# Kernel optimization log

Measured on AMD Instinct MI355X. Metric: run time of the kernel, lower is better.

## Reference

```python
import jax, jax.numpy as jnp
import numpy as np

# model dims
B, S, R, D = 2, 64, 2048, 1024      # batch, num_bars(summary len), reg seq len, embed dim
H, KVH, HD = 16, 4, 64              # q heads, kv heads, head dim
G = H // KVH                        # GQA group size
KVD = KVH * HD
TPB = R // S                        # tokens per bar = 32
SCALE = HD ** -0.5
NEG = -1e9


def _rotate_half(x):
    x1, x2 = jnp.split(x, 2, axis=-1)
    return jnp.concatenate([-x2, x1], axis=-1)


def _apply_rope(q, k, cos, sin):
    return q * cos + _rotate_half(q) * sin, k * cos + _rotate_half(k) * sin


def _rope_1d(seq_len):
    # standard RoPE tables, shape (1, 1, seq_len, HD)
    inv = 1.0 / (10000.0 ** (jnp.arange(0, HD, 2, dtype=jnp.float32) / HD))
    freqs = jnp.arange(seq_len, dtype=jnp.float32)[:, None] * inv
    emb = jnp.concatenate([freqs, freqs], axis=-1)
    return jnp.cos(emb)[None, None], jnp.sin(emb)[None, None]


def _rope_2d(bar_ids, tib):
    # hierarchical 2D RoPE: half the rotary freqs encode bar id, half encode token-in-bar id
    q4 = HD // 4
    inv = 1.0 / (10000.0 ** (jnp.arange(q4, dtype=jnp.float32) * 2.0 / (HD // 2)))
    fb = bar_ids.astype(jnp.float32)[..., None] * inv   # (B, R, HD/4)
    ft = tib.astype(jnp.float32)[..., None] * inv       # (B, R, HD/4)
    freqs = jnp.concatenate([fb, ft], axis=-1)          # (B, R, HD/2)
    emb = jnp.concatenate([freqs, freqs], axis=-1)      # (B, R, HD)
    return jnp.cos(emb)[:, None], jnp.sin(emb)[:, None]


def _attn(q, k, v, mask):
    # masked softmax attention; mask (Lq, Lk) broadcast over batch/heads
    s = jnp.einsum('bhqd,bhkd->bhqk', q, k) * SCALE
    s = jnp.where(mask[None, None], s, NEG)
    p = jax.nn.softmax(s, axis=-1)
    return jnp.einsum('bhqk,bhkd->bhqd', p, v)


def _lin(x, w, b):
    return x @ w + b


def _heads(x, n):
    b, l, _ = x.shape
    return x.reshape(b, l, n, HD).transpose(0, 2, 1, 3)


def _merge(x):
    b, h, l, _ = x.shape
    return x.transpose(0, 2, 1, 3).reshape(b, l, h * HD)


PARAM_SHAPES = [('w_sq', (D, D)), ('b_sq', (D,)), ('w_sk', (D, KVD)), ('b_sk', (KVD,)),
                ('w_sv', (D, KVD)), ('b_sv', (KVD,)), ('w_so', (D, D)), ('b_so', (D,)),
                ('w_rq', (D, D)), ('b_rq', (D,)), ('w_rk', (D, KVD)), ('b_rk', (KVD,)),
                ('w_rv', (D, KVD)), ('b_rv', (KVD,)), ('w_ro', (D, D)), ('b_ro', (D,)),
                ('w_k2', (D, KVD)), ('b_k2', (KVD,)), ('w_v2', (D, KVD)), ('b_v2', (KVD,))]


def setup_inputs() -> dict:
    key = jax.random.key(0)
    ks = jax.random.split(key, 2 + len(PARAM_SHAPES))
    inp = {}
    inp['sum_x'] = jax.random.normal(ks[0], (B, S, D), jnp.float32)
    inp['reg_x'] = jax.random.normal(ks[1], (B, R, D), jnp.float32)
    for i, (n, shp) in enumerate(PARAM_SHAPES):
        inp[n] = jax.random.normal(ks[2 + i], shp, jnp.float32) * 0.02
    pos = jnp.arange(R)
    bar = pos // TPB
    tib = pos % TPB
    inp['bar_ids'] = jnp.tile(bar[None], (B, 1)).astype(jnp.int32)
    inp['token_in_bar_ids'] = jnp.tile(tib[None], (B, 1)).astype(jnp.int32)
    # summarize phase: summary-bar i attends to summary j<=i and regular tokens in bars<=i
    key_bar = jnp.concatenate([jnp.arange(S), bar])
    inp['summarize_block_mask'] = key_bar[None, :] <= jnp.arange(S)[:, None]
    # updating phase: regular token t attends to summary-K2 of bars<=bar(t) and regular s<=t
    upd = jnp.concatenate([jnp.arange(S)[None, :] <= bar[:, None],
                           pos[None, :] <= pos[:, None]], axis=1)
    inp['updating_block_mask'] = upd
    return inp


def reference(sum_x, reg_x, w_sq, b_sq, w_sk, b_sk, w_sv, b_sv, w_so, b_so,
              w_rq, b_rq, w_rk, b_rk, w_rv, b_rv, w_ro, b_ro, w_k2, b_k2, w_v2, b_v2,
              summarize_block_mask, updating_block_mask, bar_ids, token_in_bar_ids):
    sum_q = _heads(_lin(sum_x, w_sq, b_sq), H)
    sum_k = _heads(_lin(sum_x, w_sk, b_sk), KVH)
    sum_v = _heads(_lin(sum_x, w_sv, b_sv), KVH)
    reg_q = _heads(_lin(reg_x, w_rq, b_rq), H)
    reg_k = _heads(_lin(reg_x, w_rk, b_rk), KVH)
    reg_v = _heads(_lin(reg_x, w_rv, b_rv), KVH)
    # 1D RoPE for summary tokens, 2D hierarchical RoPE for regular tokens
    cos, sin = _rope_1d(S)
    sum_q, sum_k = _apply_rope(sum_q, sum_k, cos, sin)
    rcos, rsin = _rope_2d(bar_ids, token_in_bar_ids)
    reg_q, reg_k = _apply_rope(reg_q, reg_k, rcos, rsin)
    rep = lambda t: jnp.repeat(t, G, axis=1)  # GQA repeat_interleave over heads
    reg_k_r, reg_v_r = rep(reg_k), rep(reg_v)
    # phase 1: summarize (summary queries over [summary; regular] keys)
    cat_k = jnp.concatenate([rep(sum_k), reg_k_r], axis=2)
    cat_v = jnp.concatenate([rep(sum_v), reg_v_r], axis=2)
    sum_attn = _merge(_attn(sum_q, cat_k, cat_v, summarize_block_mask))  # (B, S, D)
    # phase 2: updating (regular queries over [summary K2/V2; regular] keys)
    k2 = rep(_heads(_lin(sum_attn, w_k2, b_k2), KVH))
    v2 = rep(_heads(_lin(sum_attn, w_v2, b_v2), KVH))
    cat_k2 = jnp.concatenate([k2, reg_k_r], axis=2)
    cat_v2 = jnp.concatenate([v2, reg_v_r], axis=2)
    reg_attn = _merge(_attn(reg_q, cat_k2, cat_v2, updating_block_mask))  # (B, R, D)
    return _lin(sum_attn, w_so, b_so), _lin(reg_attn, w_ro, b_ro)
```

## Files before the change

### kernel.cpp

```cpp
#include <hip/hip_runtime.h>

typedef unsigned short u16;
typedef __attribute__((ext_vector_type(8))) short s8v;
typedef __attribute__((ext_vector_type(4))) float f4v;

#define B_    2
#define S_    64
#define R_    2048
#define D_    1024
#define H_    16
#define KVH_  4
#define LOG2_10K 13.287712379549449f
#define QSC_  0.18033688011112042f

__device__ __forceinline__ u16 f2bf(float f) {
  union { float f; unsigned int i; } v; v.f = f;
  unsigned int x = v.i;
  return (u16)((x + 0x7FFFu + ((x >> 16) & 1u)) >> 16);
}
__device__ __forceinline__ u16 f2bf_ru(float f) {
  union { float f; unsigned int i; } v; v.f = f;
  return (u16)((v.i + 0x8000u) >> 16);
}

struct WT10 { const float* w[10]; u16* o[10]; int C[10]; };

__global__ __launch_bounds__(256)
void transw_k(WT10 ws)
{
  const int z = blockIdx.z;
  const int C = ws.C[z];
  const int c0 = blockIdx.x * 32, k0 = blockIdx.y * 32;
  if (c0 >= C) return;
  __shared__ float t[32][33];
  const float* w = ws.w[z];
  u16* o = ws.o[z];
  const int x = threadIdx.x & 31, y = threadIdx.x >> 5;
  #pragma unroll
  for (int j = 0; j < 4; j++)
    t[y + 8 * j][x] = w[(size_t)(k0 + y + 8 * j) * C + c0 + x];
  __syncthreads();
  #pragma unroll
  for (int j = 0; j < 4; j++)
    o[(size_t)(c0 + y + 8 * j) * 1024 + k0 + x] = f2bf(t[x][y + 8 * j]);
}

__global__ __launch_bounds__(256)
void convx_k(const float* __restrict__ xa, const float* __restrict__ xb,
             u16* __restrict__ oa, u16* __restrict__ ob)
{
  int i = (blockIdx.x * 256 + threadIdx.x) * 8;
  const float* src; u16* dst; int off;
  if (i < 131072) { src = xa; dst = oa; off = i; }
  else            { src = xb; dst = ob; off = i - 131072; }
  float4 a = *(const float4*)(src + off);
  float4 b = *(const float4*)(src + off + 4);
  s8v r;
  r[0] = (short)f2bf(a.x); r[1] = (short)f2bf(a.y);
  r[2] = (short)f2bf(a.z); r[3] = (short)f2bf(a.w);
  r[4] = (short)f2bf(b.x); r[5] = (short)f2bf(b.y);
  r[6] = (short)f2bf(b.z); r[7] = (short)f2bf(b.w);
  *(s8v*)(dst + off) = r;
}

__device__ __forceinline__ void gemm_core_db(
    const u16* __restrict__ Xrow, const u16* __restrict__ WTrow,
    u16 (*Adb)[72], u16 (*Bdb)[72], f4v (&acc)[2][4],
    int tid, int l15, int l4, int wro, int wco)
{
  s8v pa[2], pb[2];
  #pragma unroll
  for (int it = 0; it < 2; it++) {
    int seg = tid + it * 512;
    int r = seg >> 3, sg = (seg & 7) * 8;
    pa[it] = *(const s8v*)(Xrow  + (size_t)r * 1024 + sg);
    pb[it] = *(const s8v*)(WTrow + (size_t)r * 1024 + sg);
  }
  #pragma unroll
  for (int it = 0; it < 2; it++) {
    int seg = tid + it * 512;
    int r = seg >> 3, sg = (seg & 7) * 8;
    *(s8v*)&Adb[r][sg] = pa[it];
    *(s8v*)&Bdb[r][sg] = pb[it];
  }
  __syncthreads();

  #pragma unroll 2
  for (int k = 0; k < 16; k++) {
    const int off = (k & 1) * 128;
    if (k + 1 < 16) {
      const int k0 = (k + 1) * 64;
      #pragma unroll
      for (int it = 0; it < 2; it++) {
        int seg = tid + it * 512;
        int r = seg >> 3, sg = (seg & 7) * 8;
        pa[it] = *(const s8v*)(Xrow  + (size_t)r * 1024 + k0 + sg);
        pb[it] = *(const s8v*)(WTrow + (size_t)r * 1024 + k0 + sg);
      }
    }
    s8v af[2][2], bf4[4][2];
    #pragma unroll
    for (int rc = 0; rc < 2; rc++) {
      af[rc][0] = *(const s8v*)&Adb[off + wro + rc * 16 + l15][l4 * 8];
      af[rc][1] = *(const s8v*)&Adb[off + wro + rc * 16 + l15][32 + l4 * 8];
    }
    #pragma unroll
    for (int cc = 0; cc < 4; cc++) {
      bf4[cc][0] = *(const s8v*)&Bdb[off + wco + cc * 16 + l15][l4 * 8];
      bf4[cc][1] = *(const s8v*)&Bdb[off + wco + cc * 16 + l15][32 + l4 * 8];
    }
    #pragma unroll
    for (int rc = 0; rc < 2; rc++)
      #pragma unroll
      for (int cc = 0; cc < 4; cc++) {
        acc[rc][cc] = __builtin_amdgcn_mfma_f32_16x16x32_bf16(af[rc][0], bf4[cc][0], acc[rc][cc], 0, 0, 0);
        acc[rc][cc] = __builtin_amdgcn_mfma_f32_16x16x32_bf16(af[rc][1], bf4[cc][1], acc[rc][cc], 0, 0, 0);
      }
    if (k + 1 < 16) {
      const int noff = ((k + 1) & 1) * 128;
      #pragma unroll
      for (int it = 0; it < 2; it++) {
        int seg = tid + it * 512;
        int r = seg >> 3, sg = (seg & 7) * 8;
        *(s8v*)&Adb[noff + r][sg] = pa[it];
        *(s8v*)&Bdb[noff + r][sg] = pb[it];
      }
    }
    __syncthreads();
  }
}

__device__ __forceinline__ void epi_to_lds(
    const f4v (&acc)[2][4], const float* __restrict__ Bp, u16* __restrict__ Es,
    int cbr, int wro, int wco, int grb, int LB,
    int ropeMode, bool rope2d, bool sc, int l15, int l4)
{
  float bv[4];
  #pragma unroll
  for (int cc = 0; cc < 4; cc++) bv[cc] = Bp[cbr + cc * 16 + l15];

  if (ropeMode == 0) {
    #pragma unroll
    for (int rc = 0; rc < 2; rc++)
      #pragma unroll
      for (int reg = 0; reg < 4; reg++) {
        int lrow = wro + rc * 16 + l4 * 4 + reg;
        #pragma unroll
        for (int cc = 0; cc < 4; cc++)
          Es[lrow * 136 + wco + cc * 16 + l15] = f2bf(acc[rc][cc][reg] + bv[cc]);
      }
  } else {
    float step = rope2d ? (LOG2_10K / 16.f) : (LOG2_10K / 32.f);
    float inv_lo = exp2f(-(float)l15 * step);
    float inv_hi = rope2d ? inv_lo : inv_lo * exp2f(-16.f * step);
    #pragma unroll
    for (int rc = 0; rc < 2; rc++)
      #pragma unroll
      for (int reg = 0; reg < 4; reg++) {
        int lrow = wro + rc * 16 + l4 * 4 + reg;
        int grow = grb + lrow;
        int pos = grow & (LB - 1);
        int bar = pos >> 5, tib = pos & 31;
        #pragma unroll
        for (int cc = 0; cc < 4; cc++) {
          float inv = (cc & 1) ? inv_hi : inv_lo;
          float bse = rope2d ? (float)((cc & 1) ? tib : bar) : (float)pos;
          float ang = bse * inv;
          float sn, cs;
          sincosf(ang, &sn, &cs);
          float v0 = acc[rc][cc][reg] + bv[cc];
          float v1 = acc[rc][cc ^ 2][reg] + bv[cc ^ 2];
          float rot = (cc < 2) ? -v1 : v1;
          float val = v0 * cs + rot * sn;
          if (sc) val *= QSC_;
          Es[lrow * 136 + wco + cc * 16 + l15] = f2bf(val);
        }
      }
  }
}

__device__ __forceinline__ void store_tile_bf16(
    const u16* __restrict__ Es, u16* __restrict__ out,
    int grb, int c0r, int NH, int LB, int LBS, int tid)
{
  #pragma unroll
  for (int it = 0; it < 4; it++) {
    int idx = it * 512 + tid;
    int r = idx >> 4, ch = idx & 15;
    int grow = grb + r;
    int b = grow >> LBS, pos = grow & (LB - 1);
    int cg = c0r + ch * 8;
    size_t base = (((size_t)b * NH + (cg >> 6)) * LB + pos) * 64 + (cg & 63);
    *(s8v*)(out + base) = *(const s8v*)(Es + r * 136 + ch * 8);
  }
}

__device__ __forceinline__ void store_tile_vT(
    const u16* __restrict__ Es, u16* __restrict__ outT,
    int grb, int kvbase, int LB, int LBS, int tid)
{
  #pragma unroll
  for (int it = 0; it < 4; it++) {
    int idx = tid + it * 512;
    int dcol = idx & 127, rg = idx >> 7;
    int grow = grb + rg * 8;
    int b = grow >> LBS, pos = grow & (LB - 1);
    u16 tmp[8];
    #pragma unroll
    for (int j = 0; j < 8; j++) tmp[j] = Es[(rg * 8 + j) * 136 + dcol];
    u16* dst = outT + (((size_t)(b * KVH_ + kvbase + (dcol >> 6))) * 64 + (dcol & 63)) * LB + pos;
    *(s8v*)dst = *(s8v*)tmp;
  }
}

struct QkvA {
  const u16 *X, *WTs, *WTr;
  const float *b0s, *b1s, *b2s, *b0r, *b1r, *b2r;
  u16 *o0s, *o1s, *o2s, *o0r, *o1r, *o2r;
};

__global__ __launch_bounds__(512)
void qkv_k(QkvA a)
{
  int orig = blockIdx.x;
  int xcd = orig & 7, sidx = orig >> 3;
  int wg = (xcd < 4) ? (xcd * 50 + sidx) : (200 + (xcd - 4) * 49 + sidx);
  const int bx = wg % 12, by = wg / 12;
  const bool issum = (by == 0);
  const int c0 = bx * 128;

  __shared__ u16 Adb[256][72];
  __shared__ u16 Bdb[256][72];
  u16* Es = &Adb[0][0];

  const int tid  = threadIdx.x;
  const int lane = tid & 63;
  const int w    = tid >> 6;
  const int l15  = lane & 15;
  const int l4   = lane >> 4;
  const int wro  = (w >> 1) * 32;
  const int wco  = (w & 1) * 64;

  f4v acc[2][4];
  #pragma unroll
  for (int i = 0; i < 2; i++)
    #pragma unroll
    for (int j = 0; j < 4; j++) acc[i][j] = (f4v){0.f, 0.f, 0.f, 0.f};

  const u16* Xrow  = a.X + (size_t)by * 128 * 1024;
  const u16* WTrow = (issum ? a.WTs : a.WTr) + (size_t)c0 * 1024;
  gemm_core_db(Xrow, WTrow, Adb, Bdb, acc, tid, l15, l4, wro, wco);

  const int LB  = issum ? 64 : 2048;
  const int LBS = issum ? 6 : 11;
  const int grb = issum ? 0 : (by - 1) * 128;

  if (c0 < 1024) {
    epi_to_lds(acc, issum ? a.b0s : a.b0r, Es, c0 + wco, wro, wco, grb, LB, 1, !issum, true, l15, l4);
    __syncthreads();
    store_tile_bf16(Es, issum ? a.o0s : a.o0r, grb, c0, 16, LB, LBS, tid);
  } else if (c0 < 1280) {
    epi_to_lds(acc, issum ? a.b1s : a.b1r, Es, c0 - 1024 + wco, wro, wco, grb, LB, 1, !issum, false, l15, l4);
    __syncthreads();
    store_tile_bf16(Es, issum ? a.o1s : a.o1r, grb, c0 - 1024, 4, LB, LBS, tid);
  } else {
    epi_to_lds(acc, issum ? a.b2s : a.b2r, Es, c0 - 1280 + wco, wro, wco, grb, LB, 0, false, false, l15, l4);
    __syncthreads();
    store_tile_vT(Es, issum ? a.o2s : a.o2r, grb, (c0 - 1280) >> 6, LB, LBS, tid);
  }
}

__global__ __launch_bounds__(512)
void gemm_p1_k(const u16* __restrict__ X, const u16* __restrict__ WT,
               const float* __restrict__ bk2, const float* __restrict__ bv2,
               const float* __restrict__ bso,
               u16* __restrict__ k2, u16* __restrict__ v2T, float* __restrict__ outsum)
{
  const int c0 = blockIdx.x * 128;

  __shared__ u16 Adb[256][72];
  __shared__ u16 Bdb[256][72];
  u16* Es = &Adb[0][0];

  const int tid  = threadIdx.x;
  const int lane = tid & 63;
  const int w    = tid >> 6;
  const int l15  = lane & 15;
  const int l4   = lane >> 4;
  const int wro  = (w >> 1) * 32;
  const int wco  = (w & 1) * 64;

  f4v acc[2][4];
  #pragma unroll
  for (int i = 0; i < 2; i++)
    #pragma unroll
    for (int j = 0; j < 4; j++) acc[i][j] = (f4v){0.f, 0.f, 0.f, 0.f};

  gemm_core_db(X, WT + (size_t)c0 * 1024, Adb, Bdb, acc, tid, l15, l4, wro, wco);

  if (c0 < 256) {
    epi_to_lds(acc, bk2, Es, c0 + wco, wro, wco, 0, 64, 0, false, false, l15, l4);
    __syncthreads();
    store_tile_bf16(Es, k2, 0, c0, 4, 64, 6, tid);
  } else if (c0 < 512) {
    epi_to_lds(acc, bv2, Es, c0 - 256 + wco, wro, wco, 0, 64, 0, false, false, l15, l4);
    __syncthreads();
    store_tile_vT(Es, v2T, 0, (c0 - 256) >> 6, 64, 6, tid);
  } else {
    float bv[4];
    #pragma unroll
    for (int cc = 0; cc < 4; cc++) bv[cc] = bso[c0 - 512 + wco + cc * 16 + l15];
    #pragma unroll
    for (int rc = 0; rc < 2; rc++)
      #pragma unroll
      for (int reg = 0; reg < 4; reg++) {
        int row = wro + rc * 16 + l4 * 4 + reg;
        #pragma unroll
        for (int cc = 0; cc < 4; cc++)
          outsum[(size_t)row * 1024 + c0 - 512 + wco + cc * 16 + l15] = acc[rc][cc][reg] + bv[cc];
      }
  }
}

__global__ __launch_bounds__(512)
void gemm_ro_k(const u16* __restrict__ X, const u16* __restrict__ WT,
               const float* __restrict__ Bp, float* __restrict__ out)
{
  int orig = blockIdx.x;
  int wg = (orig & 7) * 32 + (orig >> 3);
  const int bx = wg & 7, by = wg >> 3;
  const int c0 = bx * 128, r0 = by * 128;

  __shared__ u16 Adb[256][72];
  __shared__ u16 Bdb[256][72];

  const int tid  = threadIdx.x;
  const int lane = tid & 63;
  const int w    = tid >> 6;
  const int l15  = lane & 15;
  const int l4   = lane >> 4;
  const int wro  = (w >> 1) * 32;
  const int wco  = (w & 1) * 64;

  f4v acc[2][4];
  #pragma unroll
  for (int i = 0; i < 2; i++)
    #pragma unroll
    for (int j = 0; j < 4; j++) acc[i][j] = (f4v){0.f, 0.f, 0.f, 0.f};

  gemm_core_db(X + (size_t)r0 * 1024, WT + (size_t)c0 * 1024, Adb, Bdb, acc,
               tid, l15, l4, wro, wco);

  float bv[4];
  #pragma unroll
  for (int cc = 0; cc < 4; cc++) bv[cc] = Bp[c0 + wco + cc * 16 + l15];
  #pragma unroll
  for (int rc = 0; rc < 2; rc++)
    #pragma unroll
    for (int reg = 0; reg < 4; reg++) {
      int row = r0 + wro + rc * 16 + l4 * 4 + reg;
      #pragma unroll
      for (int cc = 0; cc < 4; cc++)
        out[(size_t)row * 1024 + c0 + wco + cc * 16 + l15] = acc[rc][cc][reg] + bv[cc];
    }
}

template<int PHASE>
__device__ __forceinline__ void attn_tile(
    const u16 (&Kc)[64][72], const u16 (&Vc)[64][72], u16 (&Ptw)[16][72],
    const s8v& qf0, const s8v& qf1, f4v (&acc)[4],
    float& m, float& lsum, int kbase, int qw, int l15, int l4)
{
  f4v s[4];
  #pragma unroll
  for (int n = 0; n < 4; n++) {
    s8v kf0 = *(const s8v*)&Kc[n * 16 + l15][l4 * 8];
    s8v kf1 = *(const s8v*)&Kc[n * 16 + l15][32 + l4 * 8];
    f4v t = {0.f, 0.f, 0.f, 0.f};
    t = __builtin_amdgcn_mfma_f32_16x16x32_bf16(kf0, qf0, t, 0, 0, 0);
    t = __builtin_amdgcn_mfma_f32_16x16x32_bf16(kf1, qf1, t, 0, 0, 0);
    s[n] = t;
  }

  const int qrow = qw + l15;
  bool need_mask = (kbase == 0) ||
    (PHASE == 1 ? (((kbase - 1) >> 5) > qw) : ((kbase - 1) > qw));
  float tmax = -1e30f;
  if (need_mask) {
    #pragma unroll
    for (int n = 0; n < 4; n++)
      #pragma unroll
      for (int reg = 0; reg < 4; reg++) {
        int kidx = kbase + n * 16 + l4 * 4 + reg;
        bool ok;
        if (kbase == 0) ok = kidx <= ((PHASE == 1) ? qrow : (qrow >> 5));
        else { int kr = kidx - 64; ok = (PHASE == 1) ? ((kr >> 5) <= qrow) : (kr <= qrow); }
        float sv = ok ? s[n][reg] : -1e30f;
        s[n][reg] = sv;
        tmax = fmaxf(tmax, sv);
      }
  } else {
    #pragma unroll
    for (int n = 0; n < 4; n++)
      #pragma unroll
      for (int reg = 0; reg < 4; reg++) tmax = fmaxf(tmax, s[n][reg]);
  }
  tmax = fmaxf(tmax, __shfl_xor(tmax, 16));
  tmax = fmaxf(tmax, __shfl_xor(tmax, 32));

  if (__any(tmax > m)) {
    float mn = fmaxf(m, tmax);
    float f  = __builtin_amdgcn_exp2f(m - mn);
    m = mn;
    lsum *= f;
    #pragma unroll
    for (int dt = 0; dt < 4; dt++)
      #pragma unroll
      for (int reg = 0; reg < 4; reg++) acc[dt][reg] *= f;
  }
  float rsum = 0.f;
  #pragma unroll
  for (int n = 0; n < 4; n++) {
    float p0 = __builtin_amdgcn_exp2f(s[n][0] - m);
    float p1 = __builtin_amdgcn_exp2f(s[n][1] - m);
    float p2 = __builtin_amdgcn_exp2f(s[n][2] - m);
    float p3 = __builtin_amdgcn_exp2f(s[n][3] - m);
    rsum += (p0 + p1) + (p2 + p3);
    uint2 pk;
    pk.x = (unsigned)f2bf_ru(p0) | ((unsigned)f2bf_ru(p1) << 16);
    pk.y = (unsigned)f2bf_ru(p2) | ((unsigned)f2bf_ru(p3) << 16);
    *(uint2*)&Ptw[l15][n * 16 + l4 * 4] = pk;
  }
  rsum += __shfl_xor(rsum, 16);
  rsum += __shfl_xor(rsum, 32);
  lsum += rsum;

  asm volatile("s_waitcnt lgkmcnt(0)" ::: "memory");

  s8v pf0 = *(const s8v*)&Ptw[l15][l4 * 8];
  s8v pf1 = *(const s8v*)&Ptw[l15][32 + l4 * 8];
  #pragma unroll
  for (int dt = 0; dt < 4; dt++) {
    s8v vf0 = *(const s8v*)&Vc[dt * 16 + l15][l4 * 8];
    s8v vf1 = *(const s8v*)&Vc[dt * 16 + l15][32 + l4 * 8];
    acc[dt] = __builtin_amdgcn_mfma_f32_16x16x32_bf16(vf0, pf0, acc[dt], 0, 0, 0);
    acc[dt] = __builtin_amdgcn_mfma_f32_16x16x32_bf16(vf1, pf1, acc[dt], 0, 0, 0);
  }
}

__global__ __launch_bounds__(512)
void attn2_k(const u16* __restrict__ Q, const u16* __restrict__ KS,
             const u16* __restrict__ KR, const u16* __restrict__ VST,
             const u16* __restrict__ VRT, u16* __restrict__ Out)
{
  const int gid = blockIdx.x;
  const int qb  = (gid & 256) ? (15 - (gid & 15)) : (gid & 15);
  const int bh  = gid >> 4;
  const int h   = bh & 15, b = bh >> 4;
  const int q0  = qb * 128;
  const int kh  = h >> 2;

  __shared__ u16 Kt[2][64][72];
  __shared__ u16 Vt[2][64][72];
  __shared__ u16 Pt[8][16][72];

  const int tid = threadIdx.x, lane = tid & 63, w = tid >> 6;
  const int l15 = lane & 15, l4 = lane >> 4;
  const int qw  = q0 + w * 16;

  const u16* qp = Q + (((size_t)b * H_ + h) * R_ + qw + l15) * 64;
  s8v qf0 = *(const s8v*)(qp + l4 * 8);
  s8v qf1 = *(const s8v*)(qp + 32 + l4 * 8);

  f4v acc[4];
  #pragma unroll
  for (int dt = 0; dt < 4; dt++) acc[dt] = (f4v){0.f, 0.f, 0.f, 0.f};
  float m = -1e30f, lsum = 0.f;

  const int ntiles = (64 + q0 + 128) >> 6;
  const size_t bh_kv = (size_t)b * KVH_ + kh;
  const int r_ = tid >> 3, sg_ = (tid & 7) * 8;

  {
    const u16* kp = KS  + bh_kv * 4096;
    const u16* vp = VST + bh_kv * 4096;
    s8v k0 = *(const s8v*)(kp + r_ * 64 + sg_);
    s8v v0 = *(const s8v*)(vp + r_ * 64 + sg_);
    *(s8v*)&Kt[0][r_][sg_] = k0;
    *(s8v*)&Vt[0][r_][sg_] = v0;
  }
  __syncthreads();

  for (int kt = 0; kt < ntiles; kt++) {
    const int cur = kt & 1;
    const int kbase = kt * 64;
    const bool pre = (kt + 1 < ntiles);
    s8v knx, vnx;
    if (pre) {
      const u16* kp = KR  + (bh_kv * R_ + kbase) * 64;
      const u16* vp = VRT + bh_kv * 64 * R_ + kbase;
      knx = *(const s8v*)(kp + r_ * 64 + sg_);
      vnx = *(const s8v*)(vp + (size_t)r_ * R_ + sg_);
    }

    const bool active = (kbase == 0) || (kbase - 64 <= qw + 15);
    if (active)
      attn_tile<2>(Kt[cur], Vt[cur], Pt[w], qf0, qf1, acc, m, lsum,
                   kbase, qw, l15, l4);

    if (pre) {
      *(s8v*)&Kt[cur ^ 1][r_][sg_] = knx;
      *(s8v*)&Vt[cur ^ 1][r_][sg_] = vnx;
    }
    __syncthreads();
  }

  float linv = 1.f / lsum;
  u16* o = Out + ((size_t)b * R_ + qw + l15) * D_ + h * 64;
  #pragma unroll
  for (int dt = 0; dt < 4; dt++) {
    ushort4 t4;
    t4.x = f2bf(acc[dt][0] * linv);
    t4.y = f2bf(acc[dt][1] * linv);
    t4.z = f2bf(acc[dt][2] * linv);
    t4.w = f2bf(acc[dt][3] * linv);
    *(ushort4*)(o + dt * 16 + l4 * 4) = t4;
  }
}

__global__ __launch_bounds__(256)
void attn1_k(const u16* __restrict__ Q, const u16* __restrict__ KS,
             const u16* __restrict__ KR, const u16* __restrict__ VST,
             const u16* __restrict__ VRT,
             float* __restrict__ pO, float* __restrict__ pml)
{
  const int gid = blockIdx.x;
  const int ck  = gid & 7;
  const int bh  = gid >> 3;
  const int h   = bh & 15, b = bh >> 4;
  const int kh  = h >> 2;
  const int kt0 = (ck * 33) >> 3;
  const int kt1 = ((ck + 1) * 33) >> 3;

  __shared__ u16 Kt[2][64][72];
  __shared__ u16 Vt[2][64][72];
  __shared__ u16 Pt[4][16][72];

  const int tid = threadIdx.x, lane = tid & 63, w = tid >> 6;
  const int l15 = lane & 15, l4 = lane >> 4;
  const int qw  = w * 16;

  const u16* qp = Q + (((size_t)b * H_ + h) * S_ + qw + l15) * 64;
  s8v qf0 = *(const s8v*)(qp + l4 * 8);
  s8v qf1 = *(const s8v*)(qp + 32 + l4 * 8);

  f4v acc[4];
  #pragma unroll
  for (int dt = 0; dt < 4; dt++) acc[dt] = (f4v){0.f, 0.f, 0.f, 0.f};
  float m = -1e30f, lsum = 0.f;

  const size_t bh_kv = (size_t)b * KVH_ + kh;
  const int r_ = tid >> 3, sg_ = (tid & 7) * 8;

  {
    const u16 *kp, *vp; int vstr;
    if (kt0 == 0) { kp = KS + bh_kv * 4096; vp = VST + bh_kv * 4096; vstr = 64; }
    else {
      kp = KR  + (bh_kv * R_ + kt0 * 64 - 64) * 64;
      vp = VRT + bh_kv * 64 * R_ + (kt0 * 64 - 64);
      vstr = R_;
    }
    s8v ka0 = *(const s8v*)(kp + r_ * 64 + sg_);
    s8v ka1 = *(const s8v*)(kp + (r_ + 32) * 64 + sg_);
    s8v va0 = *(const s8v*)(vp + (size_t)r_ * vstr + sg_);
    s8v va1 = *(const s8v*)(vp + (size_t)(r_ + 32) * vstr + sg_);
    *(s8v*)&Kt[0][r_][sg_]      = ka0;
    *(s8v*)&Kt[0][r_ + 32][sg_] = ka1;
    *(s8v*)&Vt[0][r_][sg_]      = va0;
    *(s8v*)&Vt[0][r_ + 32][sg_] = va1;
  }
  __syncthreads();

  for (int kt = kt0; kt < kt1; kt++) {
    const int cur = (kt - kt0) & 1;
    const int kbase = kt * 64;
    const bool pre = (kt + 1 < kt1);
    s8v ka0, ka1, va0, va1;
    if (pre) {
      const u16* kp = KR  + (bh_kv * R_ + kbase) * 64;
      const u16* vp = VRT + bh_kv * 64 * R_ + kbase;
      ka0 = *(const s8v*)(kp + r_ * 64 + sg_);
      ka1 = *(const s8v*)(kp + (r_ + 32) * 64 + sg_);
      va0 = *(const s8v*)(vp + (size_t)r_ * R_ + sg_);
      va1 = *(const s8v*)(vp + (size_t)(r_ + 32) * R_ + sg_);
    }

    const bool active = (kbase == 0) || (((kbase - 64) >> 5) <= qw + 15);
    if (active)
      attn_tile<1>(Kt[cur], Vt[cur], Pt[w], qf0, qf1, acc, m, lsum,
                   kbase, qw, l15, l4);

    if (pre) {
      *(s8v*)&Kt[cur ^ 1][r_][sg_]      = ka0;
      *(s8v*)&Kt[cur ^ 1][r_ + 32][sg_] = ka1;
      *(s8v*)&Vt[cur ^ 1][r_][sg_]      = va0;
      *(s8v*)&Vt[cur ^ 1][r_ + 32][sg_] = va1;
    }
    __syncthreads();
  }

  float* po = pO + (((size_t)ck * 32 + bh) * 64 + qw + l15) * 64;
  #pragma unroll
  for (int dt = 0; dt < 4; dt++)
    *(f4v*)(po + dt * 16 + l4 * 4) = acc[dt];
  if (l4 == 0) {
    float* pm = pml + (((size_t)ck * 32 + bh) * 64 + qw + l15) * 2;
    pm[0] = m; pm[1] = lsum;
  }
}

__global__ __launch_bounds__(256)
void comb1_k(const float* __restrict__ pO, const float* __restrict__ pml,
             u16* __restrict__ sattn)
{
  const int bh = blockIdx.x;
  const int b = bh >> 4, h = bh & 15;
  const int q  = threadIdx.x >> 2;
  const int d0 = (threadIdx.x & 3) * 16;
  float mv[8], lv[8], mstar = -1e30f;
  #pragma unroll
  for (int c = 0; c < 8; c++) {
    const float* p = pml + (((size_t)c * 32 + bh) * 64 + q) * 2;
    mv[c] = p[0]; lv[c] = p[1];
    mstar = fmaxf(mstar, mv[c]);
  }
  float o[16];
  #pragma unroll
  for (int j = 0; j < 16; j++) o[j] = 0.f;
  float lsum = 0.f;
  #pragma unroll
  for (int c = 0; c < 8; c++) {
    float wgt = __builtin_amdgcn_exp2f(mv[c] - mstar);
    lsum += lv[c] * wgt;
    const float* po = pO + (((size_t)c * 32 + bh) * 64 + q) * 64 + d0;
    #pragma unroll
    for (int j = 0; j < 16; j++) o[j] += po[j] * wgt;
  }
  float inv = 1.f / lsum;
  u16 ob[16];
  #pragma unroll
  for (int j = 0; j < 16; j++) ob[j] = f2bf(o[j] * inv);
  u16* out = sattn + ((size_t)(b * 64 + q)) * 1024 + h * 64 + d0;
  *(s8v*)out       = *(s8v*)&ob[0];
  *(s8v*)(out + 8) = *(s8v*)&ob[8];
}

extern "C" void kernel_launch(void* const* d_in, const int* in_sizes, int n_in,
                              void* d_out, int out_size, void* d_ws, size_t ws_size,
                              hipStream_t stream)
{
  (void)out_size; (void)ws_size;

  static const int expect[22] = {
    131072, 4194304,
    1048576, 1024, 262144, 256,
    262144, 256, 1048576, 1024,
    1048576, 1024, 262144, 256,
    262144, 256, 1048576, 1024,
    262144, 256, 262144, 256
  };
  if (n_in < 22) return;
  for (int i = 0; i < 22; i++) if (in_sizes[i] != expect[i]) return;

  const float* sum_x = (const float*)d_in[0];
  const float* reg_x = (const float*)d_in[1];
  const float* w_sq = (const float*)d_in[2];  const float* b_sq = (const float*)d_in[3];
  const float* w_sk = (const float*)d_in[4];  const float* b_sk = (const float*)d_in[5];
  const float* w_sv = (const float*)d_in[6];  const float* b_sv = (const float*)d_in[7];
  const float* w_so = (const float*)d_in[8];  const float* b_so = (const float*)d_in[9];
  const float* w_rq = (const float*)d_in[10]; const float* b_rq = (const float*)d_in[11];
  const float* w_rk = (const float*)d_in[12]; const float* b_rk = (const float*)d_in[13];
  const float* w_rv = (const float*)d_in[14]; const float* b_rv = (const float*)d_in[15];
  const float* w_ro = (const float*)d_in[16]; const float* b_ro = (const float*)d_in[17];
  const float* w_k2 = (const float*)d_in[18]; const float* b_k2 = (const float*)d_in[19];
  const float* w_v2 = (const float*)d_in[20]; const float* b_v2 = (const float*)d_in[21];

  u16* ws    = (u16*)d_ws;
  u16* xs_bf = ws;
  u16* xr_bf = xs_bf + 131072;
  u16* wt_s  = xr_bf + 4194304;
  u16* wt_r  = wt_s  + 1572864;
  u16* wt_p  = wt_r  + 1572864;
  u16* wt_ro = wt_p  + 1572864;
  u16* sq    = wt_ro + 1048576;
  u16* sk    = sq    + 131072;
  u16* svT   = sk    + 32768;
  u16* rq    = svT   + 32768;
  u16* rk    = rq    + 4194304;
  u16* rvT   = rk    + 1048576;
  u16* sattn = rvT   + 1048576;
  u16* k2    = sattn + 131072;
  u16* v2T   = k2    + 32768;
  u16* rattn = v2T   + 32768;

  float* pO  = (float*)rattn;
  float* pml = pO + 1048576;

  float* out_sum = (float*)d_out;
  float* out_reg = out_sum + 131072;

  dim3 blk(256);

  WT10 wt;
  wt.w[0] = w_sq; wt.o[0] = wt_s;              wt.C[0] = 1024;
  wt.w[1] = w_rq; wt.o[1] = wt_r;              wt.C[1] = 1024;
  wt.w[2] = w_so; wt.o[2] = wt_p + 512 * 1024; wt.C[2] = 1024;
  wt.w[3] = w_ro; wt.o[3] = wt_ro;             wt.C[3] = 1024;
  wt.w[4] = w_sk; wt.o[4] = wt_s + 1024 * 1024; wt.C[4] = 256;
  wt.w[5] = w_sv; wt.o[5] = wt_s + 1280 * 1024; wt.C[5] = 256;
  wt.w[6] = w_rk; wt.o[6] = wt_r + 1024 * 1024; wt.C[6] = 256;
  wt.w[7] = w_rv; wt.o[7] = wt_r + 1280 * 1024; wt.C[7] = 256;
  wt.w[8] = w_k2; wt.o[8] = wt_p;               wt.C[8] = 256;
  wt.w[9] = w_v2; wt.o[9] = wt_p + 256 * 1024;  wt.C[9] = 256;
  transw_k<<<dim3(32, 32, 10), blk, 0, stream>>>(wt);
  convx_k<<<dim3(2112), blk, 0, stream>>>(sum_x, reg_x, xs_bf, xr_bf);

  QkvA qa;
  qa.X = xs_bf; qa.WTs = wt_s; qa.WTr = wt_r;
  qa.b0s = b_sq; qa.b1s = b_sk; qa.b2s = b_sv;
  qa.b0r = b_rq; qa.b1r = b_rk; qa.b2r = b_rv;
  qa.o0s = sq; qa.o1s = sk; qa.o2s = svT;
  qa.o0r = rq; qa.o1r = rk; qa.o2r = rvT;
  qkv_k<<<dim3(396), dim3(512), 0, stream>>>(qa);

  attn1_k<<<dim3(256), blk, 0, stream>>>(sq, sk, rk, svT, rvT, pO, pml);
  comb1_k<<<dim3(32), blk, 0, stream>>>(pO, pml, sattn);

  gemm_p1_k<<<dim3(12), dim3(512), 0, stream>>>(sattn, wt_p, b_k2, b_v2, b_so, k2, v2T, out_sum);

  attn2_k<<<dim3(512), dim3(512), 0, stream>>>(rq, k2, rk, v2T, rvT, rattn);

  gemm_ro_k<<<dim3(256), dim3(512), 0, stream>>>(rattn, wt_ro, b_ro, out_reg);
}
```

Baseline: 135.9 us.

## Process two query strips per wave in attn2, fuse conversion kernel, add setprio

```diff
diff --git a/kernel.cpp b/kernel.cpp
--- a/kernel.cpp
+++ b/kernel.cpp
@@ -23,12 +23,43 @@
   return (u16)((v.i + 0x8000u) >> 16);
 }
 
+__device__ __forceinline__ f4v mfma2(const s8v& a0, const s8v& a1,
+                                     const s8v& b0, const s8v& b1) {
+  f4v t = {0.f, 0.f, 0.f, 0.f};
+  t = __builtin_amdgcn_mfma_f32_16x16x32_bf16(a0, b0, t, 0, 0, 0);
+  t = __builtin_amdgcn_mfma_f32_16x16x32_bf16(a1, b1, t, 0, 0, 0);
+  return t;
+}
+
 struct WT10 { const float* w[10]; u16* o[10]; int C[10]; };
 
 __global__ __launch_bounds__(256)
-void transw_k(WT10 ws)
+void transw_k(WT10 ws, const float* __restrict__ xa, const float* __restrict__ xb,
+              u16* __restrict__ oa, u16* __restrict__ ob)
 {
   const int z = blockIdx.z;
+  if (z == 10) {
+    int gid = blockIdx.x + blockIdx.y * 32;
+    #pragma unroll
+    for (int it = 0; it < 3; it++) {
+      int idx = gid * 256 + threadIdx.x + it * 262144;
+      if (idx < 540672) {
+        int i = idx * 8;
+        const float* src; u16* dst; int off;
+        if (i < 131072) { src = xa; dst = oa; off = i; }
+        else            { src = xb; dst = ob; off = i - 131072; }
+        float4 a = *(const float4*)(src + off);
+        float4 b = *(const float4*)(src + off + 4);
+        s8v r;
+        r[0] = (short)f2bf(a.x); r[1] = (short)f2bf(a.y);
+        r[2] = (short)f2bf(a.z); r[3] = (short)f2bf(a.w);
+        r[4] = (short)f2bf(b.x); r[5] = (short)f2bf(b.y);
+        r[6] = (short)f2bf(b.z); r[7] = (short)f2bf(b.w);
+        *(s8v*)(dst + off) = r;
+      }
+    }
+    return;
+  }
   const int C = ws.C[z];
   const int c0 = blockIdx.x * 32, k0 = blockIdx.y * 32;
   if (c0 >= C) return;
@@ -43,24 +74,6 @@
   #pragma unroll
   for (int j = 0; j < 4; j++)
     o[(size_t)(c0 + y + 8 * j) * 1024 + k0 + x] = f2bf(t[x][y + 8 * j]);
-}
-
-__global__ __launch_bounds__(256)
-void convx_k(const float* __restrict__ xa, const float* __restrict__ xb,
-             u16* __restrict__ oa, u16* __restrict__ ob)
-{
-  int i = (blockIdx.x * 256 + threadIdx.x) * 8;
-  const float* src; u16* dst; int off;
-  if (i < 131072) { src = xa; dst = oa; off = i; }
-  else            { src = xb; dst = ob; off = i - 131072; }
-  float4 a = *(const float4*)(src + off);
-  float4 b = *(const float4*)(src + off + 4);
-  s8v r;
-  r[0] = (short)f2bf(a.x); r[1] = (short)f2bf(a.y);
-  r[2] = (short)f2bf(a.z); r[3] = (short)f2bf(a.w);
-  r[4] = (short)f2bf(b.x); r[5] = (short)f2bf(b.y);
-  r[6] = (short)f2bf(b.z); r[7] = (short)f2bf(b.w);
-  *(s8v*)(dst + off) = r;
 }
 
 __device__ __forceinline__ void gemm_core_db(
@@ -366,25 +379,10 @@
 }
 
 template<int PHASE>
-__device__ __forceinline__ void attn_tile(
-    const u16 (&Kc)[64][72], const u16 (&Vc)[64][72], u16 (&Ptw)[16][72],
-    const s8v& qf0, const s8v& qf1, f4v (&acc)[4],
-    float& m, float& lsum, int kbase, int qw, int l15, int l4)
-{
-  f4v s[4];
-  #pragma unroll
-  for (int n = 0; n < 4; n++) {
-    s8v kf0 = *(const s8v*)&Kc[n * 16 + l15][l4 * 8];
-    s8v kf1 = *(const s8v*)&Kc[n * 16 + l15][32 + l4 * 8];
-    f4v t = {0.f, 0.f, 0.f, 0.f};
-    t = __builtin_amdgcn_mfma_f32_16x16x32_bf16(kf0, qf0, t, 0, 0, 0);
-    t = __builtin_amdgcn_mfma_f32_16x16x32_bf16(kf1, qf1, t, 0, 0, 0);
-    s[n] = t;
-  }
-
-  const int qrow = qw + l15;
-  bool need_mask = (kbase == 0) ||
-    (PHASE == 1 ? (((kbase - 1) >> 5) > qw) : ((kbase - 1) > qw));
+__device__ __forceinline__ void strip_sm(
+    f4v (&s)[4], float& m, float& lsum, f4v (&acc)[4],
+    u16 (&PtS)[16][72], bool need_mask, int kbase, int qrow, int l15, int l4)
+{
   float tmax = -1e30f;
   if (need_mask) {
     #pragma unroll
@@ -429,26 +427,14 @@
     uint2 pk;
     pk.x = (unsigned)f2bf_ru(p0) | ((unsigned)f2bf_ru(p1) << 16);
     pk.y = (unsigned)f2bf_ru(p2) | ((unsigned)f2bf_ru(p3) << 16);
-    *(uint2*)&Ptw[l15][n * 16 + l4 * 4] = pk;
+    *(uint2*)&PtS[l15][n * 16 + l4 * 4] = pk;
   }
   rsum += __shfl_xor(rsum, 16);
   rsum += __shfl_xor(rsum, 32);
   lsum += rsum;
-
-  asm volatile("s_waitcnt lgkmcnt(0)" ::: "memory");
-
-  s8v pf0 = *(const s8v*)&Ptw[l15][l4 * 8];
-  s8v pf1 = *(const s8v*)&Ptw[l15][32 + l4 * 8];
-  #pragma unroll
-  for (int dt = 0; dt < 4; dt++) {
-    s8v vf0 = *(const s8v*)&Vc[dt * 16 + l15][l4 * 8];
-    s8v vf1 = *(const s8v*)&Vc[dt * 16 + l15][32 + l4 * 8];
-    acc[dt] = __builtin_amdgcn_mfma_f32_16x16x32_bf16(vf0, pf0, acc[dt], 0, 0, 0);
-    acc[dt] = __builtin_amdgcn_mfma_f32_16x16x32_bf16(vf1, pf1, acc[dt], 0, 0, 0);
-  }
-}
-
-__global__ __launch_bounds__(512)
+}
+
+__global__ __launch_bounds__(256)
 void attn2_k(const u16* __restrict__ Q, const u16* __restrict__ KS,
              const u16* __restrict__ KR, const u16* __restrict__ VST,
              const u16* __restrict__ VRT, u16* __restrict__ Out)
@@ -466,28 +452,37 @@
 
   const int tid = threadIdx.x, lane = tid & 63, w = tid >> 6;
   const int l15 = lane & 15, l4 = lane >> 4;
-  const int qw  = q0 + w * 16;
-
-  const u16* qp = Q + (((size_t)b * H_ + h) * R_ + qw + l15) * 64;
-  s8v qf0 = *(const s8v*)(qp + l4 * 8);
-  s8v qf1 = *(const s8v*)(qp + 32 + l4 * 8);
-
-  f4v acc[4];
-  #pragma unroll
-  for (int dt = 0; dt < 4; dt++) acc[dt] = (f4v){0.f, 0.f, 0.f, 0.f};
-  float m = -1e30f, lsum = 0.f;
+  const int qw0 = q0 + w * 16;
+  const int qw1 = qw0 + 64;
+
+  const u16* qp0 = Q + (((size_t)b * H_ + h) * R_ + qw0 + l15) * 64;
+  const u16* qp1 = Q + (((size_t)b * H_ + h) * R_ + qw1 + l15) * 64;
+  s8v qfa0 = *(const s8v*)(qp0 + l4 * 8), qfa1 = *(const s8v*)(qp0 + 32 + l4 * 8);
+  s8v qfb0 = *(const s8v*)(qp1 + l4 * 8), qfb1 = *(const s8v*)(qp1 + 32 + l4 * 8);
+
+  f4v acc0[4], acc1[4];
+  #pragma unroll
+  for (int dt = 0; dt < 4; dt++) {
+    acc0[dt] = (f4v){0.f, 0.f, 0.f, 0.f};
+    acc1[dt] = (f4v){0.f, 0.f, 0.f, 0.f};
+  }
+  float m0 = -1e30f, ls0 = 0.f, m1 = -1e30f, ls1 = 0.f;
 
   const int ntiles = (64 + q0 + 128) >> 6;
   const size_t bh_kv = (size_t)b * KVH_ + kh;
-  const int r_ = tid >> 3, sg_ = (tid & 7) * 8;
 
   {
     const u16* kp = KS  + bh_kv * 4096;
     const u16* vp = VST + bh_kv * 4096;
-    s8v k0 = *(const s8v*)(kp + r_ * 64 + sg_);
-    s8v v0 = *(const s8v*)(vp + r_ * 64 + sg_);
-    *(s8v*)&Kt[0][r_][sg_] = k0;
-    *(s8v*)&Vt[0][r_][sg_] = v0;
+    #pragma unroll
+    for (int it = 0; it < 2; it++) {
+      int idx = tid + it * 256;
+      int r = idx >> 3, sg = (idx & 7) * 8;
+      s8v kv = *(const s8v*)(kp + r * 64 + sg);
+      s8v vv = *(const s8v*)(vp + r * 64 + sg);
+      *(s8v*)&Kt[0][r][sg] = kv;
+      *(s8v*)&Vt[0][r][sg] = vv;
+    }
   }
   __syncthreads();
 
@@ -495,36 +490,86 @@
     const int cur = kt & 1;
     const int kbase = kt * 64;
     const bool pre = (kt + 1 < ntiles);
-    s8v knx, vnx;
+    s8v knx[2], vnx[2];
     if (pre) {
       const u16* kp = KR  + (bh_kv * R_ + kbase) * 64;
       const u16* vp = VRT + bh_kv * 64 * R_ + kbase;
-      knx = *(const s8v*)(kp + r_ * 64 + sg_);
-      vnx = *(const s8v*)(vp + (size_t)r_ * R_ + sg_);
-    }
-
-    const bool active = (kbase == 0) || (kbase - 64 <= qw + 15);
-    if (active)
-      attn_tile<2>(Kt[cur], Vt[cur], Pt[w], qf0, qf1, acc, m, lsum,
-                   kbase, qw, l15, l4);
+      #pragma unroll
+      for (int it = 0; it < 2; it++) {
+        int idx = tid + it * 256;
+        int r = idx >> 3, sg = (idx & 7) * 8;
+        knx[it] = *(const s8v*)(kp + r * 64 + sg);
+        vnx[it] = *(const s8v*)(vp + (size_t)r * R_ + sg);
+      }
+    }
+
+    const bool act0 = (kbase == 0) || (kbase - 64 <= qw0 + 15);
+
+    f4v s0[4], s1[4];
+    __builtin_amdgcn_s_setprio(1);
+    #pragma unroll
+    for (int n = 0; n < 4; n++) {
+      s8v kf0 = *(const s8v*)&Kt[cur][n * 16 + l15][l4 * 8];
+      s8v kf1 = *(const s8v*)&Kt[cur][n * 16 + l15][32 + l4 * 8];
+      if (act0) s0[n] = mfma2(kf0, kf1, qfa0, qfa1);
+      s1[n] = mfma2(kf0, kf1, qfb0, qfb1);
+    }
+    __builtin_amdgcn_s_setprio(0);
+
+    bool nm0 = (kbase == 0) || ((kbase - 1) > qw0);
+    bool nm1 = (kbase == 0) || ((kbase - 1) > qw1);
+    if (act0) strip_sm<2>(s0, m0, ls0, acc0, Pt[w],     nm0, kbase, qw0 + l15, l15, l4);
+    strip_sm<2>(s1, m1, ls1, acc1, Pt[w + 4], nm1, kbase, qw1 + l15, l15, l4);
+
+    asm volatile("s_waitcnt lgkmcnt(0)" ::: "memory");
+
+    s8v pfa0, pfa1;
+    if (act0) {
+      pfa0 = *(const s8v*)&Pt[w][l15][l4 * 8];
+      pfa1 = *(const s8v*)&Pt[w][l15][32 + l4 * 8];
+    }
+    s8v pfb0 = *(const s8v*)&Pt[w + 4][l15][l4 * 8];
+    s8v pfb1 = *(const s8v*)&Pt[w + 4][l15][32 + l4 * 8];
+
+    __builtin_amdgcn_s_setprio(1);
+    #pragma unroll
+    for (int dt = 0; dt < 4; dt++) {
+      s8v vf0 = *(const s8v*)&Vt[cur][dt * 16 + l15][l4 * 8];
+      s8v vf1 = *(const s8v*)&Vt[cur][dt * 16 + l15][32 + l4 * 8];
+      if (act0) {
+        acc0[dt] = __builtin_amdgcn_mfma_f32_16x16x32_bf16(vf0, pfa0, acc0[dt], 0, 0, 0);
+        acc0[dt] = __builtin_amdgcn_mfma_f32_16x16x32_bf16(vf1, pfa1, acc0[dt], 0, 0, 0);
+      }
+      acc1[dt] = __builtin_amdgcn_mfma_f32_16x16x32_bf16(vf0, pfb0, acc1[dt], 0, 0, 0);
+      acc1[dt] = __builtin_amdgcn_mfma_f32_16x16x32_bf16(vf1, pfb1, acc1[dt], 0, 0, 0);
+    }
+    __builtin_amdgcn_s_setprio(0);
 
     if (pre) {
-      *(s8v*)&Kt[cur ^ 1][r_][sg_] = knx;
-      *(s8v*)&Vt[cur ^ 1][r_][sg_] = vnx;
+      #pragma unroll
+      for (int it = 0; it < 2; it++) {
+        int idx = tid + it * 256;
+        int r = idx >> 3, sg = (idx & 7) * 8;
+        *(s8v*)&Kt[cur ^ 1][r][sg] = knx[it];
+        *(s8v*)&Vt[cur ^ 1][r][sg] = vnx[it];
+      }
     }
     __syncthreads();
   }
 
-  float linv = 1.f / lsum;
-  u16* o = Out + ((size_t)b * R_ + qw + l15) * D_ + h * 64;
+  float li0 = 1.f / ls0, li1 = 1.f / ls1;
+  u16* o0 = Out + ((size_t)b * R_ + qw0 + l15) * D_ + h * 64;
+  u16* o1 = Out + ((size_t)b * R_ + qw1 + l15) * D_ + h * 64;
   #pragma unroll
   for (int dt = 0; dt < 4; dt++) {
     ushort4 t4;
-    t4.x = f2bf(acc[dt][0] * linv);
-    t4.y = f2bf(acc[dt][1] * linv);
-    t4.z = f2bf(acc[dt][2] * linv);
-    t4.w = f2bf(acc[dt][3] * linv);
-    *(ushort4*)(o + dt * 16 + l4 * 4) = t4;
+    t4.x = f2bf(acc0[dt][0] * li0); t4.y = f2bf(acc0[dt][1] * li0);
+    t4.z = f2bf(acc0[dt][2] * li0); t4.w = f2bf(acc0[dt][3] * li0);
+    *(ushort4*)(o0 + dt * 16 + l4 * 4) = t4;
+    ushort4 u4;
+    u4.x = f2bf(acc1[dt][0] * li1); u4.y = f2bf(acc1[dt][1] * li1);
+    u4.z = f2bf(acc1[dt][2] * li1); u4.w = f2bf(acc1[dt][3] * li1);
+    *(ushort4*)(o1 + dt * 16 + l4 * 4) = u4;
   }
 }
 
@@ -596,9 +641,31 @@
     }
 
     const bool active = (kbase == 0) || (((kbase - 64) >> 5) <= qw + 15);
-    if (active)
-      attn_tile<1>(Kt[cur], Vt[cur], Pt[w], qf0, qf1, acc, m, lsum,
-                   kbase, qw, l15, l4);
+    if (active) {
+      f4v s[4];
+      __builtin_amdgcn_s_setprio(1);
+      #pragma unroll
+      for (int n = 0; n < 4; n++) {
+        s8v kf0 = *(const s8v*)&Kt[cur][n * 16 + l15][l4 * 8];
+        s8v kf1 = *(const s8v*)&Kt[cur][n * 16 + l15][32 + l4 * 8];
+        s[n] = mfma2(kf0, kf1, qf0, qf1);
+      }
+      __builtin_amdgcn_s_setprio(0);
+      bool nm = (kbase == 0) || (((kbase - 1) >> 5) > qw);
+      strip_sm<1>(s, m, lsum, acc, Pt[w], nm, kbase, qw + l15, l15, l4);
+      asm volatile("s_waitcnt lgkmcnt(0)" ::: "memory");
+      s8v pf0 = *(const s8v*)&Pt[w][l15][l4 * 8];
+      s8v pf1 = *(const s8v*)&Pt[w][l15][32 + l4 * 8];
+      __builtin_amdgcn_s_setprio(1);
+      #pragma unroll
+      for (int dt = 0; dt < 4; dt++) {
+        s8v vf0 = *(const s8v*)&Vt[cur][dt * 16 + l15][l4 * 8];
+        s8v vf1 = *(const s8v*)&Vt[cur][dt * 16 + l15][32 + l4 * 8];
+        acc[dt] = __builtin_amdgcn_mfma_f32_16x16x32_bf16(vf0, pf0, acc[dt], 0, 0, 0);
+        acc[dt] = __builtin_amdgcn_mfma_f32_16x16x32_bf16(vf1, pf1, acc[dt], 0, 0, 0);
+      }
+      __builtin_amdgcn_s_setprio(0);
+    }
 
     if (pre) {
       *(s8v*)&Kt[cur ^ 1][r_][sg_]      = ka0;
@@ -722,8 +789,7 @@
   wt.w[7] = w_rv; wt.o[7] = wt_r + 1280 * 1024; wt.C[7] = 256;
   wt.w[8] = w_k2; wt.o[8] = wt_p;               wt.C[8] = 256;
   wt.w[9] = w_v2; wt.o[9] = wt_p + 256 * 1024;  wt.C[9] = 256;
-  transw_k<<<dim3(32, 32, 10), blk, 0, stream>>>(wt);
-  convx_k<<<dim3(2112), blk, 0, stream>>>(sum_x, reg_x, xs_bf, xr_bf);
+  transw_k<<<dim3(32, 32, 11), blk, 0, stream>>>(wt, sum_x, reg_x, xs_bf, xr_bf);
 
   QkvA qa;
   qa.X = xs_bf; qa.WTs = wt_s; qa.WTr = wt_r;
@@ -738,7 +804,7 @@
 
   gemm_p1_k<<<dim3(12), dim3(512), 0, stream>>>(sattn, wt_p, b_k2, b_v2, b_so, k2, v2T, out_sum);
 
-  attn2_k<<<dim3(512), dim3(512), 0, stream>>>(rq, k2, rk, v2T, rvT, rattn);
+  attn2_k<<<dim3(512), dim3(256), 0, stream>>>(rq, k2, rk, v2T, rvT, rattn);
 
   gemm_ro_k<<<dim3(256), dim3(512), 0, stream>>>(rattn, wt_ro, b_ro, out_reg);
 }
```

Result: slower. 158.5 us (+16.6%).
